# Kernel tuning notes

Measured on AMD Instinct MI355X. Metric: run time of the kernel, lower is better.

Reference implementation:

```python
import jax, jax.numpy as jnp
import numpy as np

GROUP_SIZE = 16
OUT_FEATURES = 8192
IN_FEATURES = 8192


def block_dequantize_min_bit(x_quant_packed, normalization):
    """Unpack 3-bit values (8 values per 3 bytes) and dequantize per-group.

    x_quant_packed: [n_groups, group_size*3//8] int (byte values 0..255)
    normalization:  [n_groups, 1] float
    returns flat float32 vector of length n_groups*group_size.
    """
    normalization = normalization.astype(jnp.float32)
    packed_width = x_quant_packed.shape[1]
    group_size = packed_width * 8 // 3
    b = x_quant_packed.astype(jnp.int32).reshape(-1, 3)
    b0, b1, b2 = b[:, 0], b[:, 1], b[:, 2]
    v0 = (b0 >> 5) & 7
    v1 = (b0 >> 2) & 7
    v2 = ((b0 & 3) << 1) | ((b1 >> 7) & 1)
    v3 = (b1 >> 4) & 7
    v4 = (b1 >> 1) & 7
    v5 = ((b1 & 1) << 2) | ((b2 >> 6) & 3)
    v6 = (b2 >> 3) & 7
    v7 = b2 & 7
    unpacked = jnp.stack([v0, v1, v2, v3, v4, v5, v6, v7], axis=1)  # [-1, 8]
    x_quant = unpacked.reshape(-1, group_size).astype(jnp.float32)
    x_norm = x_quant / 7.0
    x = x_norm * 2.0 * normalization - normalization
    return x.reshape(-1)


def setup_inputs() -> dict:
    key = jax.random.key(0)
    k1, k2, k3, k4 = jax.random.split(key, 4)
    n_groups = OUT_FEATURES * IN_FEATURES // GROUP_SIZE
    x = jax.random.normal(k1, (64, IN_FEATURES), dtype=jnp.float32)
    weight_q3 = jax.random.randint(k2, (n_groups, GROUP_SIZE * 3 // 8), 0, 256, dtype=jnp.int32)
    # positive per-group max-abs scales (quantizer stores abs().max())
    weight_norm = jax.random.uniform(k3, (n_groups, 1), dtype=jnp.float32, minval=0.01, maxval=1.0)
    bias = jax.random.normal(k4, (OUT_FEATURES,), dtype=jnp.float32)
    return {"x": x, "weight_q3": weight_q3, "weight_norm": weight_norm, "bias": bias}


def reference(x, weight_q3, weight_norm, bias):
    w = block_dequantize_min_bit(weight_q3, weight_norm).reshape(OUT_FEATURES, IN_FEATURES)
    # F.linear: y = x @ W^T + b
    return jnp.einsum('bi,oi->bo', x, w) + bias
```

## Files before the change

kernel.cpp:

```cpp
#include <hip/hip_runtime.h>
#include <hip/hip_bf16.h>


#define BATCH   64
#define IN_F    8192
#define OUT_F   8192

#define PK_BYTES 12288
#define PN_BYTES 2048
#define PA_BYTES 8192
#define BUF_BYTES (PK_BYTES + PN_BYTES + PA_BYTES)

typedef __attribute__((ext_vector_type(8))) short bf16x8;
typedef __attribute__((ext_vector_type(4))) float f32x4;

__device__ __forceinline__ ushort f2bf(float f) {
  union { float f; unsigned u; } a; a.f = f;
  unsigned r = a.u + 0x7fffu + ((a.u >> 16) & 1u);
  return (ushort)(r >> 16);
}

__device__ __forceinline__ void gl_lds16(const void* g, void* l) {
  __builtin_amdgcn_global_load_lds((const __attribute__((address_space(1))) void*)g,
                                   (__attribute__((address_space(3))) void*)l, 16, 0, 0);
}
__device__ __forceinline__ void gl_lds4(const void* g, void* l) {
  __builtin_amdgcn_global_load_lds((const __attribute__((address_space(1))) void*)g,
                                   (__attribute__((address_space(3))) void*)l, 4, 0, 0);
}

__global__ void __launch_bounds__(256) xcvt_kernel(const float* __restrict__ x,
                                                   ushort* __restrict__ xb) {
  int i = blockIdx.x * 256 + threadIdx.x;
  float4 v = ((const float4*)x)[i];
  ushort4 o;
  o.x = f2bf(v.x); o.y = f2bf(v.y); o.z = f2bf(v.z); o.w = f2bf(v.w);
  ((ushort4*)xb)[i] = o;
}

__device__ __forceinline__ bf16x8 dqfrag(int b0, int b1, int b2, float nrm) {
  float c1 = nrm * (2.0f / 7.0f);
  float c0 = nrm;
  int v0 = (b0 >> 5) & 7;
  int v1 = (b0 >> 2) & 7;
  int v2 = ((b0 & 3) << 1) | ((b1 >> 7) & 1);
  int v3 = (b1 >> 4) & 7;
  int v4 = (b1 >> 1) & 7;
  int v5 = ((b1 & 1) << 2) | ((b2 >> 6) & 3);
  int v6 = (b2 >> 3) & 7;
  int v7 = b2 & 7;
  union { __hip_bfloat162 h[4]; bf16x8 v; } r;
  r.h[0] = __float22bfloat162_rn(make_float2(fmaf((float)v0, c1, -c0), fmaf((float)v1, c1, -c0)));
  r.h[1] = __float22bfloat162_rn(make_float2(fmaf((float)v2, c1, -c0), fmaf((float)v3, c1, -c0)));
  r.h[2] = __float22bfloat162_rn(make_float2(fmaf((float)v4, c1, -c0), fmaf((float)v5, c1, -c0)));
  r.h[3] = __float22bfloat162_rn(make_float2(fmaf((float)v6, c1, -c0), fmaf((float)v7, c1, -c0)));
  return r.v;
}

template <int KS>
__global__ void __launch_bounds__(256) gemm3b_kernel(const ushort* __restrict__ xb,
                                                     const int* __restrict__ wq,
                                                     const float* __restrict__ wnorm,
                                                     float* __restrict__ partial) {
  constexpr int K_SLICE = IN_F / KS;
  constexpr int NTILE = K_SLICE / 64;

  __shared__ __align__(16) char LDS[2][BUF_BYTES];

  const int tid  = threadIdx.x;
  const int lane = tid & 63;
  const int w    = tid >> 6;
  const int l15  = lane & 15;
  const int h    = lane >> 4;
  const int nb128 = blockIdx.x * 128;
  const int s    = blockIdx.y;
  const int kbase = s * K_SLICE;
  const int kg0   = kbase >> 4;

  const char*  wqp = (const char*)wq + (size_t)nb128 * 12288 + (size_t)kg0 * 24;
  const float* wnp = wnorm + (size_t)nb128 * 512 + kg0;
  const char*  xbp = (const char*)xb + (size_t)kbase * 2;

  f32x4 acc[2][4];
  #pragma unroll
  for (int n = 0; n < 2; ++n)
    #pragma unroll
    for (int m = 0; m < 4; ++m) acc[n][m] = (f32x4){0.f, 0.f, 0.f, 0.f};

#define STAGE(BUF, KT)                                                        \
  do {                                                                        \
          \
    _Pragma("unroll")                                                         \
    for (int i = 0; i < 3; ++i) {                                             \
      int t = tid * 16 + i * 4096;                                            \
      int row = (int)(((unsigned)t * 43691u) >> 22);                          \
      int off = t - row * 96;                                                 \
      gl_lds16(wqp + (size_t)row * 12288 + (KT) * 96 + off,                   \
               &LDS[BUF][i * 4096 + w * 1024]);                               \
    }                                                                         \
                                               \
    _Pragma("unroll")                                                         \
    for (int i = 0; i < 2; ++i) {                                             \
      int t2 = tid * 4 + i * 1024;                                            \
      int row = t2 >> 4;                                                      \
      int g = (t2 >> 2) & 3;                                                  \
      gl_lds4(wnp + (size_t)row * 512 + (KT) * 4 + g,                         \
              &LDS[BUF][PK_BYTES + i * 1024 + w * 256]);                      \
    }                                                                         \
             \
    _Pragma("unroll")                                                         \
    for (int i = 0; i < 2; ++i) {                                             \
      int t = tid * 16 + i * 4096;                                            \
      int row = t >> 7;                                                       \
      int s16 = (t >> 4) & 7;                                                 \
      int c16 = s16 ^ (row & 7);                                              \
      gl_lds16(xbp + (size_t)row * (IN_F * 2) + (KT) * 128 + c16 * 16,        \
               &LDS[BUF][PK_BYTES + PN_BYTES + i * 4096 + w * 1024]);         \
    }                                                                         \
  } while (0)

#define COMPUTE(BUF)                                                          \
  do {                                                                        \
    const char*  pk  = &LDS[BUF][0];                                          \
    const float* pnf = (const float*)&LDS[BUF][PK_BYTES];                     \
    const char*  pa  = &LDS[BUF][PK_BYTES + PN_BYTES];                        \
    _Pragma("unroll")                                                         \
    for (int ks = 0; ks < 2; ++ks) {                                          \
      bf16x8 af[4];                                                           \
      _Pragma("unroll")                                                       \
      for (int m = 0; m < 4; ++m) {                                           \
        int row = m * 16 + l15;                                               \
        int cch = ks * 4 + h;                                                 \
        af[m] = *(const bf16x8*)(pa + row * 128 + ((cch ^ (row & 7)) * 16));  \
      }                                                                       \
      bf16x8 bfr[2];                                                          \
      _Pragma("unroll")                                                       \
      for (int n = 0; n < 2; ++n) {                                           \
        int r = w * 32 + n * 16 + l15;                                        \
        int g = ks * 2 + (h >> 1);                                            \
        const uint* p = (const uint*)(pk + r * 96 + g * 24 + (h & 1) * 12);   \
        bfr[n] = dqfrag(p[0], p[1], p[2], pnf[r * 4 + g]);                    \
      }                                                                       \
      _Pragma("unroll")                                                       \
      for (int m = 0; m < 4; ++m)                                             \
        _Pragma("unroll")                                                     \
        for (int n = 0; n < 2; ++n)                                           \
          acc[n][m] = __builtin_amdgcn_mfma_f32_16x16x32_bf16(af[m], bfr[n],  \
                                                              acc[n][m], 0, 0, 0); \
    }                                                                         \
  } while (0)

  STAGE(0, 0);
  __syncthreads();

  for (int kt = 0; kt < NTILE; kt += 2) {
    if (kt + 1 < NTILE) STAGE(1, kt + 1);
    COMPUTE(0);
    __syncthreads();
    if (kt + 2 < NTILE) STAGE(0, kt + 2);
    COMPUTE(1);
    __syncthreads();
  }

#undef STAGE
#undef COMPUTE

  float* pout = partial + (size_t)s * BATCH * OUT_F;
  const int nb = nb128 + w * 32;
  #pragma unroll
  for (int n = 0; n < 2; ++n) {
    int col = nb + n * 16 + l15;
    #pragma unroll
    for (int m = 0; m < 4; ++m) {
      int rowb = m * 16 + h * 4;
      #pragma unroll
      for (int r = 0; r < 4; ++r)
        pout[(size_t)(rowb + r) * OUT_F + col] = acc[n][m][r];
    }
  }
}

template <int KS>
__global__ void __launch_bounds__(256) reduce_kernel(const float* __restrict__ partial,
                                                     const float* __restrict__ bias,
                                                     float* __restrict__ out) {
  int i = blockIdx.x * 256 + threadIdx.x;
  float4 a = ((const float4*)partial)[i];
  #pragma unroll
  for (int s2 = 1; s2 < KS; ++s2) {
    float4 b = ((const float4*)partial)[i + s2 * (BATCH * OUT_F / 4)];
    a.x += b.x; a.y += b.y; a.z += b.z; a.w += b.w;
  }
  float4 bv = ((const float4*)bias)[i & (OUT_F / 4 - 1)];
  a.x += bv.x; a.y += bv.y; a.z += bv.z; a.w += bv.w;
  ((float4*)out)[i] = a;
}

extern "C" void kernel_launch(void* const* d_in, const int* in_sizes, int n_in,
                              void* d_out, int out_size, void* d_ws, size_t ws_size,
                              hipStream_t stream) {
  const float* x     = (const float*)d_in[0];
  const int*   wq    = (const int*)d_in[1];
  const float* wnorm = (const float*)d_in[2];
  const float* bias  = (const float*)d_in[3];
  float* out = (float*)d_out;

  const size_t xb_bytes = (size_t)BATCH * IN_F * 2;
  ushort* xb      = (ushort*)d_ws;
  float*  partial = (float*)((char*)d_ws + xb_bytes);

  hipLaunchKernelGGL(xcvt_kernel, dim3(BATCH * IN_F / 4 / 256), dim3(256), 0, stream, x, xb);

  const size_t slice_bytes = (size_t)BATCH * OUT_F * 4;
  if (ws_size >= xb_bytes + 8 * slice_bytes) {
    hipLaunchKernelGGL((gemm3b_kernel<8>), dim3(OUT_F / 128, 8), dim3(256), 0, stream,
                       xb, wq, wnorm, partial);
    hipLaunchKernelGGL((reduce_kernel<8>), dim3(BATCH * OUT_F / 4 / 256), dim3(256), 0, stream,
                       partial, bias, out);
  } else {
    hipLaunchKernelGGL((gemm3b_kernel<4>), dim3(OUT_F / 128, 4), dim3(256), 0, stream,
                       xb, wq, wnorm, partial);
    hipLaunchKernelGGL((reduce_kernel<4>), dim3(BATCH * OUT_F / 4 / 256), dim3(256), 0, stream,
                       partial, bias, out);
  }
}
```

Before: 44.40 us.

## Halve N-tile, preload group scales into LDS, single-barrier pipeline, more K splits

The GEMM tile is narrowed from 128 to 64 output columns per block, with one 16-column fragment per wave. All per-group scales for the block's K-slice are preloaded into a dedicated LDS array up front, replacing the per-tile 4-byte async scale loads. The double-buffer loop now uses one barrier per tile instead of two and is fully unrolled, and a 16-way K split is added when workspace allows. This raises block count and occupancy for a memory-bound dequant GEMM. In exchange, the activation tile is reloaded twice as often per weight byte, and the 16-way split makes the reduction kernel read and write more partial sums.

```diff
diff --git a/kernel.cpp b/kernel.cpp
--- a/kernel.cpp
+++ b/kernel.cpp
@@ -6,10 +6,9 @@
 #define IN_F    8192
 #define OUT_F   8192
 
-#define PK_BYTES 12288
-#define PN_BYTES 2048
+#define PK_BYTES 6144
 #define PA_BYTES 8192
-#define BUF_BYTES (PK_BYTES + PN_BYTES + PA_BYTES)
+#define BUF_BYTES (PK_BYTES + PA_BYTES)
 
 typedef __attribute__((ext_vector_type(8))) short bf16x8;
 typedef __attribute__((ext_vector_type(4))) float f32x4;
@@ -23,10 +22,6 @@
 __device__ __forceinline__ void gl_lds16(const void* g, void* l) {
   __builtin_amdgcn_global_load_lds((const __attribute__((address_space(1))) void*)g,
                                    (__attribute__((address_space(3))) void*)l, 16, 0, 0);
-}
-__device__ __forceinline__ void gl_lds4(const void* g, void* l) {
-  __builtin_amdgcn_global_load_lds((const __attribute__((address_space(1))) void*)g,
-                                   (__attribute__((address_space(3))) void*)l, 4, 0, 0);
 }
 
 __global__ void __launch_bounds__(256) xcvt_kernel(const float* __restrict__ x,
@@ -63,67 +58,71 @@
                                                      const float* __restrict__ wnorm,
                                                      float* __restrict__ partial) {
   constexpr int K_SLICE = IN_F / KS;
-  constexpr int NTILE = K_SLICE / 64;
-
-  __shared__ __align__(16) char LDS[2][BUF_BYTES];
+  constexpr int NTILE   = K_SLICE / 64;
+  constexpr int NGROW   = K_SLICE / 16;
+
+  __shared__ __align__(16) char  LDS[2][BUF_BYTES];
+  __shared__ __align__(16) float NRM[64 * NGROW];
 
   const int tid  = threadIdx.x;
   const int lane = tid & 63;
   const int w    = tid >> 6;
   const int l15  = lane & 15;
   const int h    = lane >> 4;
-  const int nb128 = blockIdx.x * 128;
+  const int nb64 = blockIdx.x * 64;
   const int s    = blockIdx.y;
   const int kbase = s * K_SLICE;
   const int kg0   = kbase >> 4;
 
-  const char*  wqp = (const char*)wq + (size_t)nb128 * 12288 + (size_t)kg0 * 24;
-  const float* wnp = wnorm + (size_t)nb128 * 512 + kg0;
+  const char*  wqp = (const char*)wq + (size_t)nb64 * 12288 + (size_t)kg0 * 24;
+  const float* wnp = wnorm + (size_t)nb64 * 512 + kg0;
   const char*  xbp = (const char*)xb + (size_t)kbase * 2;
 
-  f32x4 acc[2][4];
-  #pragma unroll
-  for (int n = 0; n < 2; ++n)
+  f32x4 acc[4];
+  #pragma unroll
+  for (int m = 0; m < 4; ++m) acc[m] = (f32x4){0.f, 0.f, 0.f, 0.f};
+
+  {
+    constexpr int ROWB = NGROW * 4;
+    constexpr int NDM  = (64 * ROWB) / 4096;
     #pragma unroll
-    for (int m = 0; m < 4; ++m) acc[n][m] = (f32x4){0.f, 0.f, 0.f, 0.f};
+    for (int i = 0; i < NDM; ++i) {
+      int t   = tid * 16 + i * 4096;
+      int row = t / ROWB;
+      int off = t % ROWB;
+      float4 v = *(const float4*)((const char*)wnp + (size_t)row * 2048 + off);
+      *(float4*)((char*)NRM + t) = v;
+    }
+  }
+
+#define STAGE_PK_CHUNK(BUF, KT, C)                                            \
+  do {                                                                        \
+    int t   = (C) * 1024 + lane * 16;                                         \
+    int row = (int)(((unsigned)t * 43691u) >> 22);                            \
+    int off = t - row * 96;                                                   \
+    gl_lds16(wqp + (size_t)row * 12288 + (KT) * 96 + off,                     \
+             &LDS[BUF][(C) * 1024]);                                          \
+  } while (0)
 
 #define STAGE(BUF, KT)                                                        \
   do {                                                                        \
-          \
-    _Pragma("unroll")                                                         \
-    for (int i = 0; i < 3; ++i) {                                             \
-      int t = tid * 16 + i * 4096;                                            \
-      int row = (int)(((unsigned)t * 43691u) >> 22);                          \
-      int off = t - row * 96;                                                 \
-      gl_lds16(wqp + (size_t)row * 12288 + (KT) * 96 + off,                   \
-               &LDS[BUF][i * 4096 + w * 1024]);                               \
-    }                                                                         \
-                                               \
+    STAGE_PK_CHUNK(BUF, KT, w);                                               \
+    if (w < 2) STAGE_PK_CHUNK(BUF, KT, 4 + w);                                \
     _Pragma("unroll")                                                         \
     for (int i = 0; i < 2; ++i) {                                             \
-      int t2 = tid * 4 + i * 1024;                                            \
-      int row = t2 >> 4;                                                      \
-      int g = (t2 >> 2) & 3;                                                  \
-      gl_lds4(wnp + (size_t)row * 512 + (KT) * 4 + g,                         \
-              &LDS[BUF][PK_BYTES + i * 1024 + w * 256]);                      \
-    }                                                                         \
-             \
-    _Pragma("unroll")                                                         \
-    for (int i = 0; i < 2; ++i) {                                             \
-      int t = tid * 16 + i * 4096;                                            \
-      int row = t >> 7;                                                       \
-      int s16 = (t >> 4) & 7;                                                 \
-      int c16 = s16 ^ (row & 7);                                              \
-      gl_lds16(xbp + (size_t)row * (IN_F * 2) + (KT) * 128 + c16 * 16,        \
-               &LDS[BUF][PK_BYTES + PN_BYTES + i * 4096 + w * 1024]);         \
+      int row = (tid >> 3) + i * 32;                                          \
+      int c   = tid & 7;                                                      \
+      int cs  = c ^ (row & 7);                                                \
+      gl_lds16(xbp + (size_t)row * (IN_F * 2) + (KT) * 128 + cs * 16,         \
+               &LDS[BUF][PK_BYTES + i * 4096 + w * 1024]);                    \
     }                                                                         \
   } while (0)
 
-#define COMPUTE(BUF)                                                          \
+#define COMPUTE(BUF, KT)                                                      \
   do {                                                                        \
-    const char*  pk  = &LDS[BUF][0];                                          \
-    const float* pnf = (const float*)&LDS[BUF][PK_BYTES];                     \
-    const char*  pa  = &LDS[BUF][PK_BYTES + PN_BYTES];                        \
+    const char* pk = &LDS[BUF][0];                                            \
+    const char* pa = &LDS[BUF][PK_BYTES];                                     \
+    const int r_loc = w * 16 + l15;                                           \
     _Pragma("unroll")                                                         \
     for (int ks = 0; ks < 2; ++ks) {                                          \
       bf16x8 af[4];                                                           \
@@ -133,50 +132,37 @@
         int cch = ks * 4 + h;                                                 \
         af[m] = *(const bf16x8*)(pa + row * 128 + ((cch ^ (row & 7)) * 16));  \
       }                                                                       \
-      bf16x8 bfr[2];                                                          \
-      _Pragma("unroll")                                                       \
-      for (int n = 0; n < 2; ++n) {                                           \
-        int r = w * 32 + n * 16 + l15;                                        \
-        int g = ks * 2 + (h >> 1);                                            \
-        const uint* p = (const uint*)(pk + r * 96 + g * 24 + (h & 1) * 12);   \
-        bfr[n] = dqfrag(p[0], p[1], p[2], pnf[r * 4 + g]);                    \
-      }                                                                       \
+      int g = ks * 2 + (h >> 1);                                              \
+      const uint* p = (const uint*)(pk + r_loc * 96 + g * 24 + (h & 1) * 12); \
+      bf16x8 bfr = dqfrag(p[0], p[1], p[2], NRM[r_loc * NGROW + (KT) * 4 + g]); \
       _Pragma("unroll")                                                       \
       for (int m = 0; m < 4; ++m)                                             \
-        _Pragma("unroll")                                                     \
-        for (int n = 0; n < 2; ++n)                                           \
-          acc[n][m] = __builtin_amdgcn_mfma_f32_16x16x32_bf16(af[m], bfr[n],  \
-                                                              acc[n][m], 0, 0, 0); \
+        acc[m] = __builtin_amdgcn_mfma_f32_16x16x32_bf16(af[m], bfr, acc[m],  \
+                                                         0, 0, 0);            \
     }                                                                         \
   } while (0)
 
   STAGE(0, 0);
-  __syncthreads();
-
-  for (int kt = 0; kt < NTILE; kt += 2) {
-    if (kt + 1 < NTILE) STAGE(1, kt + 1);
-    COMPUTE(0);
+
+  #pragma unroll
+  for (int kt = 0; kt < NTILE; ++kt) {
     __syncthreads();
-    if (kt + 2 < NTILE) STAGE(0, kt + 2);
-    COMPUTE(1);
-    __syncthreads();
+    if (kt + 1 < NTILE) STAGE((kt + 1) & 1, kt + 1);
+    COMPUTE(kt & 1, kt);
   }
 
 #undef STAGE
+#undef STAGE_PK_CHUNK
 #undef COMPUTE
 
   float* pout = partial + (size_t)s * BATCH * OUT_F;
-  const int nb = nb128 + w * 32;
-  #pragma unroll
-  for (int n = 0; n < 2; ++n) {
-    int col = nb + n * 16 + l15;
+  const int col = nb64 + w * 16 + l15;
+  #pragma unroll
+  for (int m = 0; m < 4; ++m) {
+    int rowb = m * 16 + h * 4;
     #pragma unroll
-    for (int m = 0; m < 4; ++m) {
-      int rowb = m * 16 + h * 4;
-      #pragma unroll
-      for (int r = 0; r < 4; ++r)
-        pout[(size_t)(rowb + r) * OUT_F + col] = acc[n][m][r];
-    }
+    for (int r = 0; r < 4; ++r)
+      pout[(size_t)(rowb + r) * OUT_F + col] = acc[m][r];
   }
 }
 
@@ -212,13 +198,18 @@
   hipLaunchKernelGGL(xcvt_kernel, dim3(BATCH * IN_F / 4 / 256), dim3(256), 0, stream, x, xb);
 
   const size_t slice_bytes = (size_t)BATCH * OUT_F * 4;
-  if (ws_size >= xb_bytes + 8 * slice_bytes) {
-    hipLaunchKernelGGL((gemm3b_kernel<8>), dim3(OUT_F / 128, 8), dim3(256), 0, stream,
+  if (ws_size >= xb_bytes + 16 * slice_bytes) {
+    hipLaunchKernelGGL((gemm3b_kernel<16>), dim3(OUT_F / 64, 16), dim3(256), 0, stream,
+                       xb, wq, wnorm, partial);
+    hipLaunchKernelGGL((reduce_kernel<16>), dim3(BATCH * OUT_F / 4 / 256), dim3(256), 0, stream,
+                       partial, bias, out);
+  } else if (ws_size >= xb_bytes + 8 * slice_bytes) {
+    hipLaunchKernelGGL((gemm3b_kernel<8>), dim3(OUT_F / 64, 8), dim3(256), 0, stream,
                        xb, wq, wnorm, partial);
     hipLaunchKernelGGL((reduce_kernel<8>), dim3(BATCH * OUT_F / 4 / 256), dim3(256), 0, stream,
                        partial, bias, out);
   } else {
-    hipLaunchKernelGGL((gemm3b_kernel<4>), dim3(OUT_F / 128, 4), dim3(256), 0, stream,
+    hipLaunchKernelGGL((gemm3b_kernel<4>), dim3(OUT_F / 64, 4), dim3(256), 0, stream,
                        xb, wq, wnorm, partial);
     hipLaunchKernelGGL((reduce_kernel<4>), dim3(BATCH * OUT_F / 4 / 256), dim3(256), 0, stream,
                        partial, bias, out);
```

Result: slower. 47.26 us (+6.4%).
